# Optimization experiments

Hardware: AMD Instinct MI355X
Metric: run time of the kernel (lower is better)

The kernel has to match this reference:

```python
import jax, jax.numpy as jnp
import numpy as np
from jax import lax

C = 256
HEADS = 8
AREA = 4
MLP_DIM = int(1.2 * C)  # 307


def _conv1x1(x, w, s, b):
    # x: [B,C,H,W], w: [O,C], s,b: [O]  (Conv2d 1x1 bias=False + folded BN)
    y = jnp.einsum('bchw,oc->bohw', x, w)
    return y * s[None, :, None, None] + b[None, :, None, None]


def _dwconv3x3(x, w, s, b):
    # depthwise 3x3, groups=C; w: [C,1,3,3]
    y = lax.conv_general_dilated(x, w, (1, 1), ((1, 1), (1, 1)),
                                 feature_group_count=x.shape[1],
                                 dimension_numbers=('NCHW', 'OIHW', 'NCHW'))
    return y * s[None, :, None, None] + b[None, :, None, None]


def setup_inputs() -> dict:
    key = jax.random.key(0)
    ks = jax.random.split(key, 8)
    B, H, W = 2, 64, 64
    x = jax.random.normal(ks[0], (B, C, H, W), dtype=jnp.float32)
    std = 0.02
    w_qk = jax.random.normal(ks[1], (2 * C, C), dtype=jnp.float32) * std
    w_v = jax.random.normal(ks[2], (C, C), dtype=jnp.float32) * std
    w_pe = jax.random.normal(ks[3], (C, 1, 3, 3), dtype=jnp.float32) * std
    w_proj = jax.random.normal(ks[4], (C, C), dtype=jnp.float32) * std
    w_m1 = jax.random.normal(ks[5], (MLP_DIM, C), dtype=jnp.float32) * std
    w_m2 = jax.random.normal(ks[6], (C, MLP_DIM), dtype=jnp.float32) * std
    ones = lambda n: jnp.ones((n,), jnp.float32)
    zeros = lambda n: jnp.zeros((n,), jnp.float32)
    return {
        'x': x,
        'w_qk': w_qk, 's_qk': ones(2 * C), 'b_qk': zeros(2 * C),
        'w_v': w_v, 's_v': ones(C), 'b_v': zeros(C),
        'w_pe': w_pe, 's_pe': ones(C), 'b_pe': zeros(C),
        'w_proj': w_proj, 's_proj': ones(C), 'b_proj': zeros(C),
        'w_m1': w_m1, 's_m1': ones(MLP_DIM), 'b_m1': zeros(MLP_DIM),
        'w_m2': w_m2, 's_m2': ones(C), 'b_m2': zeros(C),
    }


def _block(x, w_qk, s_qk, b_qk, w_v, s_v, b_v, w_pe, s_pe, b_pe,
           w_proj, s_proj, b_proj, w_m1, s_m1, b_m1, w_m2, s_m2, b_m2):
    B, Cc, H, W = x.shape
    N = H * W
    hd = Cc // HEADS
    scale = hd ** -0.5

    # --- AreaAttention ---
    qk = _conv1x1(x, w_qk, s_qk, b_qk).reshape(B, 2 * Cc, N)
    v4 = _conv1x1(x, w_v, s_v, b_v)                 # [B,C,H,W]
    pe = _dwconv3x3(v4, w_pe, s_pe, b_pe)           # positional encoding
    v = v4.reshape(B, Cc, N)

    # area split (row-major reshape, identical to torch contiguous reshape)
    Ba, Na = B * AREA, N // AREA
    qk = qk.reshape(Ba, 2 * Cc, Na)
    v = v.reshape(Ba, Cc, Na)
    q, k = qk[:, :Cc], qk[:, Cc:]
    q = q.reshape(Ba, HEADS, hd, Na)
    k = k.reshape(Ba, HEADS, hd, Na)
    v = v.reshape(Ba, HEADS, hd, Na)

    attn = jnp.einsum('bhdn,bhdm->bhnm', q, k) * scale  # [Ba,H,Na,Na]
    attn = jax.nn.softmax(attn, axis=-1)
    out = jnp.einsum('bhdm,bhnm->bhdn', v, attn)         # [Ba,H,hd,Na]

    out = out.reshape(B, Cc, N).reshape(B, Cc, H, W)
    attn_out = _conv1x1(out + pe, w_proj, s_proj, b_proj)

    x1 = x + attn_out  # add=True (shortcut and in_c==out_c)

    # --- conv2 MLP: Conv(SiLU) -> Conv(act=False) ---
    m = jax.nn.silu(_conv1x1(x1, w_m1, s_m1, b_m1))
    m = _conv1x1(m, w_m2, s_m2, b_m2)
    return x1 + m


def reference(x, w_qk, s_qk, b_qk, w_v, s_v, b_v, w_pe, s_pe, b_pe,
              w_proj, s_proj, b_proj, w_m1, s_m1, b_m1, w_m2, s_m2, b_m2):
    return _block(x, w_qk, s_qk, b_qk, w_v, s_v, b_v, w_pe, s_pe, b_pe,
                  w_proj, s_proj, b_proj, w_m1, s_m1, b_m1, w_m2, s_m2, b_m2)
```

## Files before the change

### kernel.cpp

```cpp
#include <hip/hip_runtime.h>

typedef __attribute__((ext_vector_type(8))) short s8v;
typedef __attribute__((ext_vector_type(4))) float f4v;

#define QSC (0.17677669529663687f * 1.4426950408889634f)

__device__ __forceinline__ unsigned short f2bf(float x) {
    unsigned u = __float_as_uint(x);
    return (unsigned short)((u + 0x7fffu + ((u >> 16) & 1u)) >> 16);
}
__device__ __forceinline__ float bf2f(unsigned short h) {
    return __uint_as_float(((unsigned)h) << 16);
}
__device__ __forceinline__ unsigned trunc2(float a, float b) {
    return (__float_as_uint(b) & 0xffff0000u) | (__float_as_uint(a) >> 16);
}

__global__ __launch_bounds__(256) void wconv_kernel(
    const float* __restrict__ wqk, const float* __restrict__ sqk, const float* __restrict__ bqk,
    const float* __restrict__ wv,  const float* __restrict__ sv,  const float* __restrict__ bv,
    const float* __restrict__ wprj, const float* __restrict__ sprj,
    const float* __restrict__ wm1, const float* __restrict__ sm1, const float* __restrict__ bm1,
    const float* __restrict__ wm2, const float* __restrict__ sm2,
    const float* __restrict__ wpe9,
    unsigned short* __restrict__ Wqkv, unsigned short* __restrict__ Wp,
    unsigned short* __restrict__ Wm1,  unsigned short* __restrict__ Wm2,
    float* __restrict__ bpad, float* __restrict__ bqv, float* __restrict__ wpeT)
{
    int i = blockIdx.x * 256 + threadIdx.x;
    if (i < 196608) {
        int o = i >> 8, c = i & 255;
        float w;
        if (o < 512) { float f = ((o & 127) < 64) ? QSC : 1.f; w = wqk[i] * sqk[o] * f; }
        else          w = wv[(o - 512) * 256 + c] * sv[o - 512];
        Wqkv[i] = f2bf(w);
    } else if (i < 262144) {
        int j = i - 196608; int o = j >> 8; Wp[j] = f2bf(wprj[j] * sprj[o]);
    } else if (i < 360448) {
        int j = i - 262144; int o = j >> 8, c = j & 255;
        Wm1[j] = (o < 307) ? f2bf(wm1[o * 256 + c] * sm1[o]) : (unsigned short)0;
    } else if (i < 458752) {
        int j = i - 360448; int o = j / 384, c = j - o * 384;
        Wm2[j] = (c < 307) ? f2bf(wm2[o * 307 + c] * sm2[o]) : (unsigned short)0;
    } else if (i < 459136) {
        int j = i - 458752; bpad[j] = (j < 307) ? bm1[j] : 0.f;
    } else if (i < 459904) {
        int j = i - 459136;
        bqv[j] = (j < 512) ? (bqk[j] * (((j & 127) < 64) ? QSC : 1.f)) : bv[j - 512];
    } else if (i < 462208) {
        int j = i - 459904; int k = j >> 8, c = j & 255;
        wpeT[j] = wpe9[c * 9 + k];
    }
}

__global__ __launch_bounds__(256) void mmqkv_kernel(
    const float* __restrict__ X, const unsigned short* __restrict__ Wb,
    const float* __restrict__ bi,
    unsigned short* __restrict__ qP, unsigned short* __restrict__ kP,
    unsigned short* __restrict__ vC, unsigned short* __restrict__ vT)
{
    __shared__ unsigned short Ap[64][40];
    __shared__ unsigned short Wt[128][40];
    const int tid = threadIdx.x, lane = tid & 63, wv = tid >> 6;
    const int lo4 = lane & 15, quad = lane >> 4;
    const int p0 = blockIdx.x * 64, o0 = blockIdx.y * 128, bB = blockIdx.z;
    const int ph = (wv & 1) * 32, oh = (wv >> 1) * 64;
    const int c2 = tid & 15, pg = tid >> 4;
    const int oW0 = tid >> 2, oW1 = (tid + 256) >> 2;
    const int cW = (tid & 3) * 8;
    const float* xb = X + (size_t)bB * 256 * 4096;

    f4v acc[4][2];
    #pragma unroll
    for (int i = 0; i < 4; i++)
        #pragma unroll
        for (int j = 0; j < 2; j++)
            acc[i][j] = (f4v){0.f, 0.f, 0.f, 0.f};

    float4 fa = *(const float4*)&xb[(size_t)(2 * c2) * 4096 + p0 + pg * 4];
    float4 fb = *(const float4*)&xb[(size_t)(2 * c2 + 1) * 4096 + p0 + pg * 4];
    uint4 wReg0 = *(const uint4*)(Wb + (size_t)(o0 + oW0) * 256 + cW);
    uint4 wReg1 = *(const uint4*)(Wb + (size_t)(o0 + oW1) * 256 + cW);

    for (int kc = 0; kc < 8; kc++) {
        __syncthreads();
        {
            float av[4] = {fa.x, fa.y, fa.z, fa.w};
            float bv2[4] = {fb.x, fb.y, fb.z, fb.w};
            #pragma unroll
            for (int i = 0; i < 4; i++)
                *(unsigned*)&Ap[pg * 4 + i][2 * c2] =
                    (unsigned)f2bf(av[i]) | ((unsigned)f2bf(bv2[i]) << 16);
        }
        *(uint4*)&Wt[oW0][cW] = wReg0;
        *(uint4*)&Wt[oW1][cW] = wReg1;
        __syncthreads();
        if (kc < 7) {
            int k1 = (kc + 1) * 32;
            fa = *(const float4*)&xb[(size_t)(k1 + 2 * c2) * 4096 + p0 + pg * 4];
            fb = *(const float4*)&xb[(size_t)(k1 + 2 * c2 + 1) * 4096 + p0 + pg * 4];
            wReg0 = *(const uint4*)(Wb + (size_t)(o0 + oW0) * 256 + k1 + cW);
            wReg1 = *(const uint4*)(Wb + (size_t)(o0 + oW1) * 256 + k1 + cW);
        }
        s8v af[4], bx[2];
        #pragma unroll
        for (int of = 0; of < 4; of++)
            af[of] = *(const s8v*)&Wt[oh + of * 16 + lo4][quad * 8];
        #pragma unroll
        for (int pf = 0; pf < 2; pf++)
            bx[pf] = *(const s8v*)&Ap[ph + pf * 16 + lo4][quad * 8];
        #pragma unroll
        for (int of = 0; of < 4; of++)
            #pragma unroll
            for (int pf = 0; pf < 2; pf++)
                acc[of][pf] = __builtin_amdgcn_mfma_f32_16x16x32_bf16(af[of], bx[pf], acc[of][pf], 0, 0, 0);
    }
    #pragma unroll
    for (int of = 0; of < 4; of++) {
        int ob = o0 + oh + of * 16 + quad * 4;
        float4 bb = *(const float4*)&bi[ob];
        float bbv[4] = {bb.x, bb.y, bb.z, bb.w};
        #pragma unroll
        for (int pf = 0; pf < 2; pf++) {
            int p = p0 + ph + pf * 16 + lo4;
            unsigned short b4[4];
            #pragma unroll
            for (int r = 0; r < 4; r++) b4[r] = f2bf(acc[of][pf][r] + bbv[r]);
            if (ob < 512) {
                int gg = ob >> 7, rr = ob & 127;
                int hh = (rr & 63) >> 3, j0 = rr & 7;
                unsigned short* dst = (rr >= 64) ? kP : qP;
                *(ushort4*)&dst[((((size_t)(bB * 4 + gg)) * 8 + hh) * 1024 + (p & 1023)) * 32
                                + (p >> 10) * 8 + j0] = *(ushort4*)b4;
            } else {
                *(ushort4*)&vC[((size_t)(bB * 4096 + p)) * 256 + (ob - 512)] = *(ushort4*)b4;
                #pragma unroll
                for (int r = 0; r < 4; r++)
                    vT[((size_t)(bB * 256 + ob - 512 + r)) * 4096 + p] = b4[r];
            }
        }
    }
}

__global__ __launch_bounds__(256) void attn_kernel(
    const unsigned short* __restrict__ qP, const unsigned short* __restrict__ kP,
    const unsigned short* __restrict__ vT,
    unsigned short* __restrict__ Opart, float* __restrict__ Lpart)
{
    __shared__ unsigned short Pq[4][32][64];
    const int tid = threadIdx.x;
    const int w = tid >> 6, lane = tid & 63;
    const int lo4 = lane & 15, quad = lane >> 4;
    const int swz = (lo4 & 7) << 4;
    const int n0 = blockIdx.z * 128;
    const int h = blockIdx.y;
    const int z = blockIdx.x;
    const int ba = z >> 2, spl = z & 3;
    const int bB = ba >> 2, g = ba & 3;
    const int mbase = spl * 256;

    const unsigned short* qb = qP + (((size_t)(bB * 4) + g) * 8 + h) * 32768;
    const unsigned short* kb = kP + (((size_t)(bB * 4) + g) * 8 + h) * 32768;

    s8v qf[2];
    #pragma unroll
    for (int qc = 0; qc < 2; qc++)
        qf[qc] = *(const s8v*)(qb + (size_t)(n0 + w * 32 + qc * 16 + lo4) * 32 + quad * 8);
    const int dd0 = lo4, dd1 = 16 + lo4;
    const unsigned short* vb0 = vT + ((size_t)(bB * 256 + g * 64 + h * 8 + (dd0 & 7))) * 4096 + (dd0 >> 3) * 1024 + mbase + quad * 8;
    const unsigned short* vb1 = vT + ((size_t)(bB * 256 + g * 64 + h * 8 + (dd1 & 7))) * 4096 + (dd1 >> 3) * 1024 + mbase + quad * 8;

    f4v oacc[2][2], Lacc[2];
    #pragma unroll
    for (int i = 0; i < 2; i++) {
        Lacc[i] = (f4v){0.f, 0.f, 0.f, 0.f};
        #pragma unroll
        for (int j = 0; j < 2; j++)
            oacc[i][j] = (f4v){0.f, 0.f, 0.f, 0.f};
    }
    s8v ones;
    #pragma unroll
    for (int j = 0; j < 8; j++) ones[j] = (short)0x3F80;

    s8v kf[4], vReg[2][2];
    #pragma unroll
    for (int mf = 0; mf < 4; mf++)
        kf[mf] = *(const s8v*)(kb + (size_t)(mbase + mf * 16 + lo4) * 32 + quad * 8);
    #pragma unroll
    for (int mc = 0; mc < 2; mc++) {
        vReg[mc][0] = *(const s8v*)(vb0 + mc * 32);
        vReg[mc][1] = *(const s8v*)(vb1 + mc * 32);
    }

    #pragma unroll
    for (int sc = 0; sc < 4; sc++) {
        s8v kfn[4], vNext[2][2];
        if (sc < 3) {
            #pragma unroll
            for (int mf = 0; mf < 4; mf++)
                kfn[mf] = *(const s8v*)(kb + (size_t)(mbase + (sc + 1) * 64 + mf * 16 + lo4) * 32 + quad * 8);
            #pragma unroll
            for (int mc = 0; mc < 2; mc++) {
                vNext[mc][0] = *(const s8v*)(vb0 + (sc + 1) * 64 + mc * 32);
                vNext[mc][1] = *(const s8v*)(vb1 + (sc + 1) * 64 + mc * 32);
            }
        }
        f4v sT[4][2];
        __builtin_amdgcn_s_setprio(1);
        #pragma unroll
        for (int mf = 0; mf < 4; mf++)
            #pragma unroll
            for (int qc = 0; qc < 2; qc++)
                sT[mf][qc] = __builtin_amdgcn_mfma_f32_16x16x32_bf16(kf[mf], qf[qc], (f4v){0.f, 0.f, 0.f, 0.f}, 0, 0, 0);
        __builtin_amdgcn_s_setprio(0);
        #pragma unroll
        for (int qc = 0; qc < 2; qc++) {
            char* prow = (char*)&Pq[w][qc * 16 + lo4][0];
            #pragma unroll
            for (int mf = 0; mf < 4; mf++) {
                float p0v = exp2f(sT[mf][qc][0]);
                float p1v = exp2f(sT[mf][qc][1]);
                float p2v = exp2f(sT[mf][qc][2]);
                float p3v = exp2f(sT[mf][qc][3]);
                uint2 pk;
                pk.x = trunc2(p0v, p1v);
                pk.y = trunc2(p2v, p3v);
                *(uint2*)(prow + ((mf * 32 + quad * 8) ^ swz)) = pk;
            }
        }
        #pragma unroll
        for (int mc = 0; mc < 2; mc++) {
            s8v pfr[2];
            #pragma unroll
            for (int qc = 0; qc < 2; qc++)
                pfr[qc] = *(const s8v*)((const char*)&Pq[w][qc * 16 + lo4][0] + ((mc * 64 + quad * 16) ^ swz));
            __builtin_amdgcn_s_setprio(1);
            #pragma unroll
            for (int df = 0; df < 2; df++)
                #pragma unroll
                for (int qc = 0; qc < 2; qc++)
                    oacc[df][qc] = __builtin_amdgcn_mfma_f32_16x16x32_bf16(vReg[mc][df], pfr[qc], oacc[df][qc], 0, 0, 0);
            #pragma unroll
            for (int qc = 0; qc < 2; qc++)
                Lacc[qc] = __builtin_amdgcn_mfma_f32_16x16x32_bf16(ones, pfr[qc], Lacc[qc], 0, 0, 0);
            __builtin_amdgcn_s_setprio(0);
        }
        if (sc < 3) {
            #pragma unroll
            for (int mf = 0; mf < 4; mf++) kf[mf] = kfn[mf];
            #pragma unroll
            for (int mc = 0; mc < 2; mc++) {
                vReg[mc][0] = vNext[mc][0];
                vReg[mc][1] = vNext[mc][1];
            }
        }
    }
    if (quad == 0) {
        size_t lb = (((size_t)(spl * 2 + bB) * 4 + g) * 8 + h) * 1024 + n0 + w * 32;
        Lpart[lb + lo4] = Lacc[0][0];
        Lpart[lb + 16 + lo4] = Lacc[1][0];
    }
    #pragma unroll
    for (int qc = 0; qc < 2; qc++)
        #pragma unroll
        for (int df = 0; df < 2; df++) {
            int pb = df * 2 + (quad >> 1);
            uint2 ov;
            ov.x = trunc2(oacc[df][qc][0], oacc[df][qc][1]);
            ov.y = trunc2(oacc[df][qc][2], oacc[df][qc][3]);
            *(uint2*)(Opart + ((size_t)(spl * 2 + bB) * 4096 + pb * 1024 + n0 + w * 32 + qc * 16 + lo4) * 256
                      + g * 64 + h * 8 + (quad & 1) * 4) = ov;
        }
}

__global__ __launch_bounds__(256) void attpe_kernel(
    const unsigned short* __restrict__ Opart, const float* __restrict__ Lpart,
    const unsigned short* __restrict__ vC, const float* __restrict__ wpeT,
    const float* __restrict__ spe, const float* __restrict__ bpe,
    unsigned short* __restrict__ attpe)
{
    int idx = blockIdx.x * 256 + threadIdx.x;
    int cg = (idx & 31) * 8;
    int p = (idx >> 5) & 4095;
    int bB = idx >> 17;
    int g = cg >> 6, h = (cg >> 3) & 7;
    int na = p & 1023;
    float L = 0.f;
    float o[8] = {};
    #pragma unroll
    for (int spl = 0; spl < 4; spl++) {
        L += Lpart[(((size_t)(spl * 2 + bB) * 4 + g) * 8 + h) * 1024 + na];
        uint4 v = *(const uint4*)(Opart + ((size_t)(spl * 2 + bB) * 4096 + p) * 256 + cg);
        unsigned short tmp[8]; *(uint4*)tmp = v;
        #pragma unroll
        for (int j = 0; j < 8; j++) o[j] += bf2f(tmp[j]);
    }
    float inv = 1.f / L;
    int hh = p >> 6, ww = p & 63;
    float pe[8] = {};
    for (int di = -1; di <= 1; di++) {
        int h2 = hh + di;
        if (h2 < 0 || h2 > 63) continue;
        for (int dj = -1; dj <= 1; dj++) {
            int w2 = ww + dj;
            if (w2 < 0 || w2 > 63) continue;
            uint4 vv = *(const uint4*)(vC + ((size_t)(bB * 4096 + h2 * 64 + w2)) * 256 + cg);
            unsigned short tmp[8]; *(uint4*)tmp = vv;
            int k = (di + 1) * 3 + (dj + 1);
            float4 wa = *(const float4*)&wpeT[k * 256 + cg];
            float4 wb = *(const float4*)&wpeT[k * 256 + cg + 4];
            float ww8[8] = {wa.x, wa.y, wa.z, wa.w, wb.x, wb.y, wb.z, wb.w};
            #pragma unroll
            for (int j = 0; j < 8; j++)
                pe[j] = fmaf(bf2f(tmp[j]), ww8[j], pe[j]);
        }
    }
    float4 sa = *(const float4*)&spe[cg];
    float4 sb = *(const float4*)&spe[cg + 4];
    float4 b0 = *(const float4*)&bpe[cg];
    float4 b1 = *(const float4*)&bpe[cg + 4];
    float sv8[8] = {sa.x, sa.y, sa.z, sa.w, sb.x, sb.y, sb.z, sb.w};
    float bv8[8] = {b0.x, b0.y, b0.z, b0.w, b1.x, b1.y, b1.z, b1.w};
    unsigned short ob[8];
    #pragma unroll
    for (int j = 0; j < 8; j++)
        ob[j] = f2bf(o[j] * inv + pe[j] * sv8[j] + bv8[j]);
    *(uint4*)(attpe + ((size_t)(bB * 4096 + p)) * 256 + cg) = *(uint4*)ob;
}

__global__ __launch_bounds__(512) void mlp3_kernel(
    const unsigned short* __restrict__ attpe, const float* __restrict__ x,
    const unsigned short* __restrict__ Wp, const float* __restrict__ bp,
    const unsigned short* __restrict__ Wm1, const float* __restrict__ bm1p,
    const unsigned short* __restrict__ Wm2, const float* __restrict__ bm2,
    float* __restrict__ out)
{
    __shared__ unsigned short bufA[16][392];
    __shared__ unsigned short bufX[16][264];
    const int tid = threadIdx.x, lane = tid & 63, wv = tid >> 6;
    const int lo4 = lane & 15, quad = lane >> 4;
    const int p0 = blockIdx.x * 16, bB = blockIdx.y;

    {
        int row = tid >> 5, cb = (tid & 31) * 8;
        *(uint4*)&bufA[row][cb] =
            *(const uint4*)(attpe + ((size_t)(bB * 4096 + p0 + row)) * 256 + cb);
    }
    __syncthreads();

    {
        f4v acc[2] = {(f4v){0.f, 0.f, 0.f, 0.f}, (f4v){0.f, 0.f, 0.f, 0.f}};
        for (int kk = 0; kk < 8; kk++) {
            s8v bx = *(const s8v*)&bufA[lo4][kk * 32 + quad * 8];
            #pragma unroll
            for (int of = 0; of < 2; of++) {
                s8v af = *(const s8v*)(Wp + (size_t)(wv * 32 + of * 16 + lo4) * 256 + kk * 32 + quad * 8);
                acc[of] = __builtin_amdgcn_mfma_f32_16x16x32_bf16(af, bx, acc[of], 0, 0, 0);
            }
        }
        #pragma unroll
        for (int of = 0; of < 2; of++) {
            int ob = wv * 32 + of * 16 + quad * 4;
            float4 bb = *(const float4*)&bp[ob];
            float bbv[4] = {bb.x, bb.y, bb.z, bb.w};
            int p = p0 + lo4;
            unsigned short b4[4];
            #pragma unroll
            for (int r = 0; r < 4; r++) {
                float y = acc[of][r] + bbv[r] + x[((size_t)(bB * 256 + ob + r)) * 4096 + p];
                b4[r] = f2bf(y);
            }
            *(ushort4*)&bufX[lo4][ob] = *(ushort4*)b4;
        }
    }
    __syncthreads();

    {
        f4v acc[3] = {(f4v){0.f, 0.f, 0.f, 0.f}, (f4v){0.f, 0.f, 0.f, 0.f}, (f4v){0.f, 0.f, 0.f, 0.f}};
        for (int kk = 0; kk < 8; kk++) {
            s8v bx = *(const s8v*)&bufX[lo4][kk * 32 + quad * 8];
            #pragma unroll
            for (int of = 0; of < 3; of++) {
                s8v af = *(const s8v*)(Wm1 + (size_t)(wv * 48 + of * 16 + lo4) * 256 + kk * 32 + quad * 8);
                acc[of] = __builtin_amdgcn_mfma_f32_16x16x32_bf16(af, bx, acc[of], 0, 0, 0);
            }
        }
        #pragma unroll
        for (int of = 0; of < 3; of++) {
            int ob = wv * 48 + of * 16 + quad * 4;
            float4 bb = *(const float4*)&bm1p[ob];
            float bbv[4] = {bb.x, bb.y, bb.z, bb.w};
            unsigned short b4[4];
            #pragma unroll
            for (int r = 0; r < 4; r++) {
                float y = acc[of][r] + bbv[r];
                y = y / (1.f + __expf(-y));
                b4[r] = f2bf(y);
            }
            *(ushort4*)&bufA[lo4][ob] = *(ushort4*)b4;
        }
    }
    __syncthreads();

    {
        f4v acc[2] = {(f4v){0.f, 0.f, 0.f, 0.f}, (f4v){0.f, 0.f, 0.f, 0.f}};
        for (int kk = 0; kk < 12; kk++) {
            s8v bx = *(const s8v*)&bufA[lo4][kk * 32 + quad * 8];
            #pragma unroll
            for (int of = 0; of < 2; of++) {
                s8v af = *(const s8v*)(Wm2 + (size_t)(wv * 32 + of * 16 + lo4) * 384 + kk * 32 + quad * 8);
                acc[of] = __builtin_amdgcn_mfma_f32_16x16x32_bf16(af, bx, acc[of], 0, 0, 0);
            }
        }
        #pragma unroll
        for (int of = 0; of < 2; of++) {
            int ob = wv * 32 + of * 16 + quad * 4;
            float4 bb = *(const float4*)&bm2[ob];
            float bbv[4] = {bb.x, bb.y, bb.z, bb.w};
            ushort4 x1v = *(const ushort4*)&bufX[lo4][ob];
            unsigned short x1a[4]; *(ushort4*)x1a = x1v;
            #pragma unroll
            for (int r = 0; r < 4; r++) {
                float y = acc[of][r] + bbv[r] + bf2f(x1a[r]);
                out[((size_t)(bB * 256 + ob + r)) * 4096 + p0 + lo4] = y;
            }
        }
    }
}

extern "C" void kernel_launch(void* const* d_in, const int* in_sizes, int n_in,
                              void* d_out, int out_size, void* d_ws, size_t ws_size,
                              hipStream_t stream)
{
    const float* x      = (const float*)d_in[0];
    const float* w_qk   = (const float*)d_in[1];
    const float* s_qk   = (const float*)d_in[2];
    const float* b_qk   = (const float*)d_in[3];
    const float* w_v    = (const float*)d_in[4];
    const float* s_v    = (const float*)d_in[5];
    const float* b_v    = (const float*)d_in[6];
    const float* w_pe   = (const float*)d_in[7];
    const float* s_pe   = (const float*)d_in[8];
    const float* b_pe   = (const float*)d_in[9];
    const float* w_proj = (const float*)d_in[10];
    const float* s_proj = (const float*)d_in[11];
    const float* b_proj = (const float*)d_in[12];
    const float* w_m1   = (const float*)d_in[13];
    const float* s_m1   = (const float*)d_in[14];
    const float* b_m1   = (const float*)d_in[15];
    const float* w_m2   = (const float*)d_in[16];
    const float* s_m2   = (const float*)d_in[17];
    const float* b_m2   = (const float*)d_in[18];
    float* out = (float*)d_out;

    const size_t NA = (size_t)2 * 4096 * 256;
    unsigned short* attpe = (unsigned short*)d_ws;
    unsigned short* vC   = attpe + NA;
    unsigned short* qP   = vC + NA;
    unsigned short* kP   = qP + NA;
    unsigned short* Opart = kP + NA;
    float* Lpart = (float*)(Opart + 4 * NA);
    unsigned short* Wqkv = (unsigned short*)(Lpart + 262144);
    unsigned short* Wp   = Wqkv + 196608;
    unsigned short* Wm1  = Wp + 65536;
    unsigned short* Wm2  = Wm1 + 98304;
    float* bpad = (float*)(Wm2 + 98304);
    float* bqv  = bpad + 384;
    float* wpeT = bqv + 768;
    unsigned short* vT = (unsigned short*)(wpeT + 2304);

    dim3 blk(256);
    wconv_kernel<<<dim3(1806), blk, 0, stream>>>(
        w_qk, s_qk, b_qk, w_v, s_v, b_v, w_proj, s_proj,
        w_m1, s_m1, b_m1, w_m2, s_m2, w_pe,
        Wqkv, Wp, Wm1, Wm2, bpad, bqv, wpeT);

    mmqkv_kernel<<<dim3(64, 6, 2), blk, 0, stream>>>(x, Wqkv, bqv, qP, kP, vC, vT);

    attn_kernel<<<dim3(32, 8, 8), blk, 0, stream>>>(qP, kP, vT, Opart, Lpart);
    attpe_kernel<<<dim3(1024), blk, 0, stream>>>(Opart, Lpart, vC, wpeT, s_pe, b_pe, attpe);

    mlp3_kernel<<<dim3(256, 2), dim3(512), 0, stream>>>(
        attpe, x, Wp, b_proj, Wm1, bpad, Wm2, b_m2, out);
}
```

Baseline: 180.0 us.

## Halve attention key split and software-pipeline PV after next QK

```diff
diff --git a/kernel.cpp b/kernel.cpp
--- a/kernel.cpp
+++ b/kernel.cpp
@@ -147,7 +147,7 @@
     const unsigned short* __restrict__ vT,
     unsigned short* __restrict__ Opart, float* __restrict__ Lpart)
 {
-    __shared__ unsigned short Pq[4][32][64];
+    __shared__ unsigned short Pq[4][2][32][64];
     const int tid = threadIdx.x;
     const int w = tid >> 6, lane = tid & 63;
     const int lo4 = lane & 15, quad = lane >> 4;
@@ -155,9 +155,9 @@
     const int n0 = blockIdx.z * 128;
     const int h = blockIdx.y;
     const int z = blockIdx.x;
-    const int ba = z >> 2, spl = z & 3;
+    const int ba = z >> 1, spl = z & 1;
     const int bB = ba >> 2, g = ba & 3;
-    const int mbase = spl * 256;
+    const int mbase = spl * 512;
 
     const unsigned short* qb = qP + (((size_t)(bB * 4) + g) * 8 + h) * 32768;
     const unsigned short* kb = kP + (((size_t)(bB * 4) + g) * 8 + h) * 32768;
@@ -182,28 +182,24 @@
     #pragma unroll
     for (int j = 0; j < 8; j++) ones[j] = (short)0x3F80;
 
-    s8v kf[4], vReg[2][2];
+    s8v kf[4], vCur[2][2];
     #pragma unroll
     for (int mf = 0; mf < 4; mf++)
         kf[mf] = *(const s8v*)(kb + (size_t)(mbase + mf * 16 + lo4) * 32 + quad * 8);
-    #pragma unroll
-    for (int mc = 0; mc < 2; mc++) {
-        vReg[mc][0] = *(const s8v*)(vb0 + mc * 32);
-        vReg[mc][1] = *(const s8v*)(vb1 + mc * 32);
-    }
-
-    #pragma unroll
-    for (int sc = 0; sc < 4; sc++) {
-        s8v kfn[4], vNext[2][2];
-        if (sc < 3) {
+
+    #pragma unroll
+    for (int sc = 0; sc < 8; sc++) {
+        s8v vNew[2][2];
+        #pragma unroll
+        for (int mc = 0; mc < 2; mc++) {
+            vNew[mc][0] = *(const s8v*)(vb0 + sc * 64 + mc * 32);
+            vNew[mc][1] = *(const s8v*)(vb1 + sc * 64 + mc * 32);
+        }
+        s8v kfn[4];
+        if (sc < 7) {
             #pragma unroll
             for (int mf = 0; mf < 4; mf++)
                 kfn[mf] = *(const s8v*)(kb + (size_t)(mbase + (sc + 1) * 64 + mf * 16 + lo4) * 32 + quad * 8);
-            #pragma unroll
-            for (int mc = 0; mc < 2; mc++) {
-                vNext[mc][0] = *(const s8v*)(vb0 + (sc + 1) * 64 + mc * 32);
-                vNext[mc][1] = *(const s8v*)(vb1 + (sc + 1) * 64 + mc * 32);
-            }
         }
         f4v sT[4][2];
         __builtin_amdgcn_s_setprio(1);
@@ -215,7 +211,7 @@
         __builtin_amdgcn_s_setprio(0);
         #pragma unroll
         for (int qc = 0; qc < 2; qc++) {
-            char* prow = (char*)&Pq[w][qc * 16 + lo4][0];
+            char* prow = (char*)&Pq[w][sc & 1][qc * 16 + lo4][0];
             #pragma unroll
             for (int mf = 0; mf < 4; mf++) {
                 float p0v = exp2f(sT[mf][qc][0]);
@@ -228,32 +224,51 @@
                 *(uint2*)(prow + ((mf * 32 + quad * 8) ^ swz)) = pk;
             }
         }
-        #pragma unroll
-        for (int mc = 0; mc < 2; mc++) {
-            s8v pfr[2];
-            #pragma unroll
-            for (int qc = 0; qc < 2; qc++)
-                pfr[qc] = *(const s8v*)((const char*)&Pq[w][qc * 16 + lo4][0] + ((mc * 64 + quad * 16) ^ swz));
-            __builtin_amdgcn_s_setprio(1);
-            #pragma unroll
-            for (int df = 0; df < 2; df++)
+        if (sc > 0) {
+            #pragma unroll
+            for (int mc = 0; mc < 2; mc++) {
+                s8v pfr[2];
                 #pragma unroll
                 for (int qc = 0; qc < 2; qc++)
-                    oacc[df][qc] = __builtin_amdgcn_mfma_f32_16x16x32_bf16(vReg[mc][df], pfr[qc], oacc[df][qc], 0, 0, 0);
+                    pfr[qc] = *(const s8v*)((const char*)&Pq[w][(sc - 1) & 1][qc * 16 + lo4][0] + ((mc * 64 + quad * 16) ^ swz));
+                __builtin_amdgcn_s_setprio(1);
+                #pragma unroll
+                for (int df = 0; df < 2; df++)
+                    #pragma unroll
+                    for (int qc = 0; qc < 2; qc++)
+                        oacc[df][qc] = __builtin_amdgcn_mfma_f32_16x16x32_bf16(vCur[mc][df], pfr[qc], oacc[df][qc], 0, 0, 0);
+                #pragma unroll
+                for (int qc = 0; qc < 2; qc++)
+                    Lacc[qc] = __builtin_amdgcn_mfma_f32_16x16x32_bf16(ones, pfr[qc], Lacc[qc], 0, 0, 0);
+                __builtin_amdgcn_s_setprio(0);
+            }
+        }
+        if (sc < 7) {
+            #pragma unroll
+            for (int mf = 0; mf < 4; mf++) kf[mf] = kfn[mf];
+        }
+        #pragma unroll
+        for (int mc = 0; mc < 2; mc++) {
+            vCur[mc][0] = vNew[mc][0];
+            vCur[mc][1] = vNew[mc][1];
+        }
+    }
+    #pragma unroll
+    for (int mc = 0; mc < 2; mc++) {
+        s8v pfr[2];
+        #pragma unroll
+        for (int qc = 0; qc < 2; qc++)
+            pfr[qc] = *(const s8v*)((const char*)&Pq[w][1][qc * 16 + lo4][0] + ((mc * 64 + quad * 16) ^ swz));
+        __builtin_amdgcn_s_setprio(1);
+        #pragma unroll
+        for (int df = 0; df < 2; df++)
             #pragma unroll
             for (int qc = 0; qc < 2; qc++)
-                Lacc[qc] = __builtin_amdgcn_mfma_f32_16x16x32_bf16(ones, pfr[qc], Lacc[qc], 0, 0, 0);
-            __builtin_amdgcn_s_setprio(0);
-        }
-        if (sc < 3) {
-            #pragma unroll
-            for (int mf = 0; mf < 4; mf++) kf[mf] = kfn[mf];
-            #pragma unroll
-            for (int mc = 0; mc < 2; mc++) {
-                vReg[mc][0] = vNext[mc][0];
-                vReg[mc][1] = vNext[mc][1];
-            }
-        }
+                oacc[df][qc] = __builtin_amdgcn_mfma_f32_16x16x32_bf16(vCur[mc][df], pfr[qc], oacc[df][qc], 0, 0, 0);
+        #pragma unroll
+        for (int qc = 0; qc < 2; qc++)
+            Lacc[qc] = __builtin_amdgcn_mfma_f32_16x16x32_bf16(ones, pfr[qc], Lacc[qc], 0, 0, 0);
+        __builtin_amdgcn_s_setprio(0);
     }
     if (quad == 0) {
         size_t lb = (((size_t)(spl * 2 + bB) * 4 + g) * 8 + h) * 1024 + n0 + w * 32;
@@ -288,7 +303,7 @@
     float L = 0.f;
     float o[8] = {};
     #pragma unroll
-    for (int spl = 0; spl < 4; spl++) {
+    for (int spl = 0; spl < 2; spl++) {
         L += Lpart[(((size_t)(spl * 2 + bB) * 4 + g) * 8 + h) * 1024 + na];
         uint4 v = *(const uint4*)(Opart + ((size_t)(spl * 2 + bB) * 4096 + p) * 256 + cg);
         unsigned short tmp[8]; *(uint4*)tmp = v;
@@ -459,8 +474,8 @@
     unsigned short* qP   = vC + NA;
     unsigned short* kP   = qP + NA;
     unsigned short* Opart = kP + NA;
-    float* Lpart = (float*)(Opart + 4 * NA);
-    unsigned short* Wqkv = (unsigned short*)(Lpart + 262144);
+    float* Lpart = (float*)(Opart + 2 * NA);
+    unsigned short* Wqkv = (unsigned short*)(Lpart + 131072);
     unsigned short* Wp   = Wqkv + 196608;
     unsigned short* Wm1  = Wp + 65536;
     unsigned short* Wm2  = Wm1 + 98304;
@@ -477,7 +492,7 @@
 
     mmqkv_kernel<<<dim3(64, 6, 2), blk, 0, stream>>>(x, Wqkv, bqv, qP, kP, vC, vT);
 
-    attn_kernel<<<dim3(32, 8, 8), blk, 0, stream>>>(qP, kP, vT, Opart, Lpart);
+    attn_kernel<<<dim3(16, 8, 8), blk, 0, stream>>>(qP, kP, vT, Opart, Lpart);
     attpe_kernel<<<dim3(1024), blk, 0, stream>>>(Opart, Lpart, vC, wpeT, s_pe, b_pe, attpe);
 
     mlp3_kernel<<<dim3(256, 2), dim3(512), 0, stream>>>(
```

Result: no change. 177.2 us (-1.6%).
